# Performance work log

Hardware: AMD Instinct MI355X
Metric: run time of the kernel (lower is better)

Reference implementation:

```python
import jax, jax.numpy as jnp
import numpy as np

N_NODES = 100000
N_NEIGH = 10
DIM = 256
N_LAYERS = 3


def setup_inputs() -> dict:
    key = jax.random.key(0)
    ks = jax.random.split(key, 8)
    x = jax.random.normal(ks[0], (N_NODES, DIM), dtype=jnp.float32)
    adj = jax.random.randint(ks[1], (N_NODES, N_NEIGH), 0, N_NODES, dtype=jnp.int32)
    # per-layer SAGE weights: Linear(2*D -> D), stored as [2D, D] for x @ W
    scale = 0.05
    W0 = jax.random.normal(ks[2], (2 * DIM, DIM), dtype=jnp.float32) * scale
    W1 = jax.random.normal(ks[3], (2 * DIM, DIM), dtype=jnp.float32) * scale
    W2 = jax.random.normal(ks[4], (2 * DIM, DIM), dtype=jnp.float32) * scale
    b0 = jnp.zeros((DIM,), dtype=jnp.float32)
    b1 = jnp.zeros((DIM,), dtype=jnp.float32)
    b2 = jnp.zeros((DIM,), dtype=jnp.float32)
    return {"x": x, "adj": adj, "W0": W0, "b0": b0, "W1": W1, "b1": b1,
            "W2": W2, "b2": b2}


def reference(x, adj, W0, b0, W1, b1, W2, b2):
    """GraphSAGE: per layer, gather sampled neighbors [N,K,D], mean over K,
    concat with self embedding, linear [2D->D], ReLU on all but last layer."""
    layers = [(W0, b0), (W1, b1), (W2, b2)]
    h = x
    for i, (W, b) in enumerate(layers):
        neigh = jnp.mean(h[adj], axis=1)                 # [N, K, D] -> [N, D]
        h = jnp.concatenate([h, neigh], axis=1) @ W + b  # [N, 2D] @ [2D, D]
        if i < len(layers) - 1:
            h = jax.nn.relu(h)
    return h
```

## Files before the change

### kernel.cpp

```cpp
#include <hip/hip_runtime.h>
#include <stdint.h>

#define NN 100000
#define NK 10
#define D  256
#define D2 512
#define MT 32

typedef short bf16x8 __attribute__((ext_vector_type(8)));
typedef float f32x4  __attribute__((ext_vector_type(4)));

__device__ __forceinline__ uint16_t f2bf(float f) {
  uint32_t u = __float_as_uint(f);
  u += 0x7fffu + ((u >> 16) & 1u);
  return (uint16_t)(u >> 16);
}
__device__ __forceinline__ uint32_t pack2(float a, float b) {
  return (uint32_t)f2bf(a) | ((uint32_t)f2bf(b) << 16);
}

__global__ __launch_bounds__(256) void quant_x(const float* __restrict__ x,
                                               uint8_t* __restrict__ q8,
                                               float*   __restrict__ qs) {
  int node = blockIdx.x * 4 + (threadIdx.x >> 6);
  int lane = threadIdx.x & 63;
  const float4 v = *(const float4*)(x + (size_t)node * D + lane * 4);
  float m = fmaxf(fmaxf(fabsf(v.x), fabsf(v.y)), fmaxf(fabsf(v.z), fabsf(v.w)));
#pragma unroll
  for (int d = 1; d < 64; d <<= 1) m = fmaxf(m, __shfl_xor(m, d, 64));
  float inv = m > 1e-30f ? 127.0f / m : 0.0f;
  int q0 = (int)rintf(v.x * inv), q1 = (int)rintf(v.y * inv);
  int q2 = (int)rintf(v.z * inv), q3 = (int)rintf(v.w * inv);
  uint32_t p = (uint32_t)(q0 & 0xff) | ((uint32_t)(q1 & 0xff) << 8) |
               ((uint32_t)(q2 & 0xff) << 16) | ((uint32_t)(q3 & 0xff) << 24);
  ((uint32_t*)(q8 + (size_t)node * D))[lane] = p;
  if (lane == 0) qs[node] = m * (1.0f / 127.0f);
}

__global__ void pack_w(const float* __restrict__ W, uint16_t* __restrict__ Wp) {
  int idx   = blockIdx.x * blockDim.x + threadIdx.x;
  int lane  = idx & 63;
  int ntile = (idx >> 6) & 15;
  int kstep = idx >> 10;
  int n  = ntile * 16 + (lane & 15);
  int k0 = kstep * 32 + (lane >> 4) * 8;
  float v[8];
#pragma unroll
  for (int j = 0; j < 8; j++) v[j] = W[(size_t)(k0 + j) * D + n];
  uint4 o;
  o.x = pack2(v[0], v[1]);
  o.y = pack2(v[2], v[3]);
  o.z = pack2(v[4], v[5]);
  o.w = pack2(v[6], v[7]);
  ((uint4*)Wp)[idx] = o;
}

template <bool SELF_F32, bool QOUT>
__global__ __launch_bounds__(256, 5) void sage_layer(
    const void*     __restrict__ hin_v,
    const uint8_t*  __restrict__ qtab,
    const float*    __restrict__ qsc,
    const int*      __restrict__ adj,
    const uint16_t* __restrict__ Wp,
    const float*    __restrict__ bias,
    void*           __restrict__ hout_v,
    uint8_t*        __restrict__ q8out,
    float*          __restrict__ qsout)
{
  __shared__ uint4 lds4[MT * 64];
  const int t  = threadIdx.x;
  const int m0 = blockIdx.x * MT;

#pragma unroll
  for (int i = 0; i < 4; i++) {
    int cidx = t + i * 256;
    int r = cidx >> 5;
    int c = cidx & 31;
    int node = m0 + r;
    uint4 o;
    if (SELF_F32) {
      const float4* p = (const float4*)((const float*)hin_v + (size_t)node * D + c * 8);
      float4 v0 = p[0], v1 = p[1];
      o.x = pack2(v0.x, v0.y); o.y = pack2(v0.z, v0.w);
      o.z = pack2(v1.x, v1.y); o.w = pack2(v1.z, v1.w);
    } else {
      o = *(const uint4*)((const uint16_t*)hin_v + (size_t)node * D + c * 8);
    }
    lds4[r * 64 + (c ^ (r & 15))] = o;
  }

  {
    const int half = t >> 5;
    const int l32  = t & 31;
#pragma unroll 1
    for (int i = 0; i < 4; i++) {
      int r = i * 8 + half;
      int node = m0 + r;
      float a0=0.f,a1=0.f,a2=0.f,a3=0.f,a4=0.f,a5=0.f,a6=0.f,a7=0.f;
#pragma unroll
      for (int k = 0; k < NK; k++) {
        int nb = adj[node * NK + k];
        float s = qsc[nb];
        uint2 v = *(const uint2*)(qtab + (size_t)nb * D + l32 * 8);
        a0 += s * (float)(int8_t)(v.x);
        a1 += s * (float)(int8_t)(v.x >> 8);
        a2 += s * (float)(int8_t)(v.x >> 16);
        a3 += s * (float)(int8_t)(v.x >> 24);
        a4 += s * (float)(int8_t)(v.y);
        a5 += s * (float)(int8_t)(v.y >> 8);
        a6 += s * (float)(int8_t)(v.y >> 16);
        a7 += s * (float)(int8_t)(v.y >> 24);
      }
      const float sc = 1.0f / (float)NK;
      uint4 o;
      o.x = pack2(a0 * sc, a1 * sc);
      o.y = pack2(a2 * sc, a3 * sc);
      o.z = pack2(a4 * sc, a5 * sc);
      o.w = pack2(a6 * sc, a7 * sc);
      int c = 32 + l32;
      lds4[r * 64 + (c ^ (r & 15))] = o;
    }
  }

  __syncthreads();

  const int w    = t >> 6;
  const int l    = t & 63;
  const int quad = l >> 4;
  const int l16  = l & 15;

  f32x4 acc[2][4];
#pragma unroll
  for (int mt = 0; mt < 2; mt++)
#pragma unroll
    for (int nt = 0; nt < 4; nt++)
      acc[mt][nt] = (f32x4){0.f, 0.f, 0.f, 0.f};

  const uint4* wp4 = (const uint4*)Wp;

#pragma unroll 2
  for (int ks = 0; ks < 16; ks++) {
    bf16x8 af[2], bfr[4];
#pragma unroll
    for (int mt = 0; mt < 2; mt++) {
      int row = mt * 16 + l16;
      int c   = ks * 4 + quad;
      af[mt] = *((const bf16x8*)&lds4[row * 64 + (c ^ (row & 15))]);
    }
#pragma unroll
    for (int nt = 0; nt < 4; nt++) {
      bfr[nt] = *((const bf16x8*)&wp4[(ks * 16 + (w * 4 + nt)) * 64 + l]);
    }
#pragma unroll
    for (int mt = 0; mt < 2; mt++)
#pragma unroll
      for (int nt = 0; nt < 4; nt++)
        acc[mt][nt] = __builtin_amdgcn_mfma_f32_16x16x32_bf16(
            af[mt], bfr[nt], acc[mt][nt], 0, 0, 0);
  }

  float lmax[2][4];
#pragma unroll
  for (int mt = 0; mt < 2; mt++)
#pragma unroll
    for (int i = 0; i < 4; i++) lmax[mt][i] = 0.0f;

#pragma unroll
  for (int mt = 0; mt < 2; mt++)
#pragma unroll
    for (int nt = 0; nt < 4; nt++)
#pragma unroll
      for (int i = 0; i < 4; i++) {
        int col = w * 64 + nt * 16 + l16;
        float v = acc[mt][nt][i] + bias[col];
        if (QOUT) v = fmaxf(v, 0.0f);
        acc[mt][nt][i] = v;
        if (QOUT) lmax[mt][i] = fmaxf(lmax[mt][i], v);
      }

  float inv[2][4];
  if (QOUT) {
#pragma unroll
    for (int d = 1; d < 16; d <<= 1)
#pragma unroll
      for (int mt = 0; mt < 2; mt++)
#pragma unroll
        for (int i = 0; i < 4; i++)
          lmax[mt][i] = fmaxf(lmax[mt][i], __shfl_xor(lmax[mt][i], d, 64));
    __syncthreads();
    float* rmax = (float*)lds4;
    if (l16 == 0) {
#pragma unroll
      for (int mt = 0; mt < 2; mt++)
#pragma unroll
        for (int i = 0; i < 4; i++)
          rmax[(mt * 16 + quad * 4 + i) * 4 + w] = lmax[mt][i];
    }
    __syncthreads();
#pragma unroll
    for (int mt = 0; mt < 2; mt++)
#pragma unroll
      for (int i = 0; i < 4; i++) {
        int row = mt * 16 + quad * 4 + i;
        float m = fmaxf(fmaxf(rmax[row * 4 + 0], rmax[row * 4 + 1]),
                        fmaxf(rmax[row * 4 + 2], rmax[row * 4 + 3]));
        inv[mt][i] = m > 1e-30f ? 127.0f / m : 0.0f;
        if (w == 0 && l16 == 0) qsout[m0 + row] = m * (1.0f / 127.0f);
      }
  }

#pragma unroll
  for (int mt = 0; mt < 2; mt++)
#pragma unroll
    for (int i = 0; i < 4; i++) {
      int rr = m0 + mt * 16 + quad * 4 + i;
#pragma unroll
      for (int nt = 0; nt < 4; nt++) {
        int col = w * 64 + nt * 16 + l16;
        float v = acc[mt][nt][i];
        if (QOUT) {
          ((uint16_t*)hout_v)[(size_t)rr * D + col] = f2bf(v);
          int q = (int)rintf(v * inv[mt][i]);
          q8out[(size_t)rr * D + col] = (uint8_t)(q & 0xff);
        } else {
          ((float*)hout_v)[(size_t)rr * D + col] = v;
        }
      }
    }
}

extern "C" void kernel_launch(void* const* d_in, const int* in_sizes, int n_in,
                              void* d_out, int out_size, void* d_ws, size_t ws_size,
                              hipStream_t stream) {
  const float* x   = (const float*)d_in[0];
  const int*   adj = (const int*)d_in[1];
  const float* W0  = (const float*)d_in[2];
  const float* b0  = (const float*)d_in[3];
  const float* W1  = (const float*)d_in[4];
  const float* b1  = (const float*)d_in[5];
  const float* W2  = (const float*)d_in[6];
  const float* b2  = (const float*)d_in[7];
  float* out = (float*)d_out;

  uint8_t*  dob = (uint8_t*)d_out;
  uint16_t* hA  = (uint16_t*)dob;
  uint8_t*  hA8 = dob + 51200000;
  uint8_t*  x8  = dob + 76800000;

  uint16_t* ws  = (uint16_t*)d_ws;
  uint16_t* Wp0 = ws;
  uint16_t* Wp1 = Wp0 + D2 * D;
  uint16_t* Wp2 = Wp1 + D2 * D;
  uint16_t* hB  = Wp2 + D2 * D;
  uint8_t*  hB8 = (uint8_t*)(hB + (size_t)NN * D);
  float*    xs  = (float*)(hB8 + (size_t)NN * D);
  float*    hAs = xs + NN;
  float*    hBs = hAs + NN;

  quant_x<<<NN / 4, 256, 0, stream>>>(x, x8, xs);
  pack_w<<<64, 256, 0, stream>>>(W0, Wp0);
  pack_w<<<64, 256, 0, stream>>>(W1, Wp1);
  pack_w<<<64, 256, 0, stream>>>(W2, Wp2);

  const int grid = NN / MT;
  sage_layer<true,  true ><<<grid, 256, 0, stream>>>(x,  x8,  xs,  adj, Wp0, b0, hA,  hA8, hAs);
  sage_layer<false, true ><<<grid, 256, 0, stream>>>(hA, hA8, hAs, adj, Wp1, b1, hB,  hB8, hBs);
  sage_layer<false, false><<<grid, 256, 0, stream>>>(hB, hB8, hBs, adj, Wp2, b2, out, nullptr, nullptr);
}
```

Baseline: 457.2 us.

## Software-pipeline neighbor gathers with double buffers and merge prep kernels

The neighbor aggregation now preloads each row's adjacency indices once, broadcasts them with shuffles, and keeps two register buffers of neighbor gathers in flight, so the loads for the next row overlap the accumulation of the current one. Self-row loads are issued before the gathers so their latency also overlaps. The input quantization and the three weight-packing kernels are merged into one launch to cut launch overhead. Occupancy is lowered from 5 to 4 blocks per unit to make room for the extra registers, which could reduce latency hiding elsewhere.

```diff
diff --git a/kernel.cpp b/kernel.cpp
--- a/kernel.cpp
+++ b/kernel.cpp
@@ -19,44 +19,53 @@
   return (uint32_t)f2bf(a) | ((uint32_t)f2bf(b) << 16);
 }
 
-__global__ __launch_bounds__(256) void quant_x(const float* __restrict__ x,
-                                               uint8_t* __restrict__ q8,
-                                               float*   __restrict__ qs) {
-  int node = blockIdx.x * 4 + (threadIdx.x >> 6);
-  int lane = threadIdx.x & 63;
-  const float4 v = *(const float4*)(x + (size_t)node * D + lane * 4);
-  float m = fmaxf(fmaxf(fabsf(v.x), fabsf(v.y)), fmaxf(fabsf(v.z), fabsf(v.w)));
-#pragma unroll
-  for (int d = 1; d < 64; d <<= 1) m = fmaxf(m, __shfl_xor(m, d, 64));
-  float inv = m > 1e-30f ? 127.0f / m : 0.0f;
-  int q0 = (int)rintf(v.x * inv), q1 = (int)rintf(v.y * inv);
-  int q2 = (int)rintf(v.z * inv), q3 = (int)rintf(v.w * inv);
-  uint32_t p = (uint32_t)(q0 & 0xff) | ((uint32_t)(q1 & 0xff) << 8) |
-               ((uint32_t)(q2 & 0xff) << 16) | ((uint32_t)(q3 & 0xff) << 24);
-  ((uint32_t*)(q8 + (size_t)node * D))[lane] = p;
-  if (lane == 0) qs[node] = m * (1.0f / 127.0f);
-}
-
-__global__ void pack_w(const float* __restrict__ W, uint16_t* __restrict__ Wp) {
-  int idx   = blockIdx.x * blockDim.x + threadIdx.x;
-  int lane  = idx & 63;
-  int ntile = (idx >> 6) & 15;
-  int kstep = idx >> 10;
-  int n  = ntile * 16 + (lane & 15);
-  int k0 = kstep * 32 + (lane >> 4) * 8;
-  float v[8];
-#pragma unroll
-  for (int j = 0; j < 8; j++) v[j] = W[(size_t)(k0 + j) * D + n];
-  uint4 o;
-  o.x = pack2(v[0], v[1]);
-  o.y = pack2(v[2], v[3]);
-  o.z = pack2(v[4], v[5]);
-  o.w = pack2(v[6], v[7]);
-  ((uint4*)Wp)[idx] = o;
+__global__ __launch_bounds__(256) void prep(
+    const float* __restrict__ x, uint8_t* __restrict__ q8, float* __restrict__ qs,
+    const float* __restrict__ W0, const float* __restrict__ W1,
+    const float* __restrict__ W2, uint16_t* __restrict__ Wp0,
+    uint16_t* __restrict__ Wp1, uint16_t* __restrict__ Wp2)
+{
+  const int bid = blockIdx.x;
+  if (bid < 192) {
+    const float* W;
+    uint16_t* Wp;
+    if (bid < 64)       { W = W0; Wp = Wp0; }
+    else if (bid < 128) { W = W1; Wp = Wp1; }
+    else                { W = W2; Wp = Wp2; }
+    int idx   = ((bid & 63) << 8) + threadIdx.x;
+    int lane  = idx & 63;
+    int ntile = (idx >> 6) & 15;
+    int kstep = idx >> 10;
+    int n  = ntile * 16 + (lane & 15);
+    int k0 = kstep * 32 + (lane >> 4) * 8;
+    float v[8];
+#pragma unroll
+    for (int j = 0; j < 8; j++) v[j] = W[(size_t)(k0 + j) * D + n];
+    uint4 o;
+    o.x = pack2(v[0], v[1]);
+    o.y = pack2(v[2], v[3]);
+    o.z = pack2(v[4], v[5]);
+    o.w = pack2(v[6], v[7]);
+    ((uint4*)Wp)[idx] = o;
+  } else {
+    int node = (bid - 192) * 4 + (threadIdx.x >> 6);
+    int lane = threadIdx.x & 63;
+    const float4 v = *(const float4*)(x + (size_t)node * D + lane * 4);
+    float m = fmaxf(fmaxf(fabsf(v.x), fabsf(v.y)), fmaxf(fabsf(v.z), fabsf(v.w)));
+#pragma unroll
+    for (int d = 1; d < 64; d <<= 1) m = fmaxf(m, __shfl_xor(m, d, 64));
+    float inv = m > 1e-30f ? 127.0f / m : 0.0f;
+    int q0 = (int)rintf(v.x * inv), q1 = (int)rintf(v.y * inv);
+    int q2 = (int)rintf(v.z * inv), q3 = (int)rintf(v.w * inv);
+    uint32_t p = (uint32_t)(q0 & 0xff) | ((uint32_t)(q1 & 0xff) << 8) |
+                 ((uint32_t)(q2 & 0xff) << 16) | ((uint32_t)(q3 & 0xff) << 24);
+    ((uint32_t*)(q8 + (size_t)node * D))[lane] = p;
+    if (lane == 0) qs[node] = m * (1.0f / 127.0f);
+  }
 }
 
 template <bool SELF_F32, bool QOUT>
-__global__ __launch_bounds__(256, 5) void sage_layer(
+__global__ __launch_bounds__(256, 4) void sage_layer(
     const void*     __restrict__ hin_v,
     const uint8_t*  __restrict__ qtab,
     const float*    __restrict__ qsc,
@@ -68,59 +77,99 @@
     float*          __restrict__ qsout)
 {
   __shared__ uint4 lds4[MT * 64];
-  const int t  = threadIdx.x;
-  const int m0 = blockIdx.x * MT;
-
-#pragma unroll
-  for (int i = 0; i < 4; i++) {
-    int cidx = t + i * 256;
-    int r = cidx >> 5;
-    int c = cidx & 31;
-    int node = m0 + r;
+  const int t    = threadIdx.x;
+  const int m0   = blockIdx.x * MT;
+  const int half = t >> 5;
+  const int l32  = t & 31;
+  const int hb   = half & ~1;
+  const int hsel = (half & 1) * 10;
+
+  int av0, av1, av2, av3;
+  {
+    const int* ap = adj + (size_t)(m0 + hb) * NK;
+    int o = (l32 < 20) ? l32 : 0;
+    av0 = ap[o];
+    av1 = ap[80 + o];
+    av2 = ap[160 + o];
+    av3 = ap[240 + o];
+  }
+
+  uint2 gA[NK], gB[NK];
+  float sA[NK], sB[NK];
+
+  auto issue = [&](int av, uint2 (&g)[NK], float (&s)[NK]) {
+#pragma unroll
+    for (int k = 0; k < NK; k++) {
+      int nb = __shfl(av, hsel + k, 32);
+      s[k] = qsc[nb];
+      g[k] = *(const uint2*)(qtab + (size_t)nb * D + l32 * 8);
+    }
+  };
+  auto consume = [&](const uint2 (&g)[NK], const float (&s)[NK], int i) {
+    int r = i * 8 + half;
+    float a0=0.f,a1=0.f,a2=0.f,a3=0.f,a4=0.f,a5=0.f,a6=0.f,a7=0.f;
+#pragma unroll
+    for (int k = 0; k < NK; k++) {
+      float sk = s[k];
+      uint2 v  = g[k];
+      a0 += sk * (float)(int8_t)(v.x);
+      a1 += sk * (float)(int8_t)(v.x >> 8);
+      a2 += sk * (float)(int8_t)(v.x >> 16);
+      a3 += sk * (float)(int8_t)(v.x >> 24);
+      a4 += sk * (float)(int8_t)(v.y);
+      a5 += sk * (float)(int8_t)(v.y >> 8);
+      a6 += sk * (float)(int8_t)(v.y >> 16);
+      a7 += sk * (float)(int8_t)(v.y >> 24);
+    }
+    const float sc = 1.0f / (float)NK;
     uint4 o;
-    if (SELF_F32) {
-      const float4* p = (const float4*)((const float*)hin_v + (size_t)node * D + c * 8);
+    o.x = pack2(a0 * sc, a1 * sc);
+    o.y = pack2(a2 * sc, a3 * sc);
+    o.z = pack2(a4 * sc, a5 * sc);
+    o.w = pack2(a6 * sc, a7 * sc);
+    int c = 32 + l32;
+    lds4[r * 64 + (c ^ (r & 15))] = o;
+  };
+
+  if constexpr (SELF_F32) {
+#pragma unroll
+    for (int i = 0; i < 4; i++) {
+      int cidx = t + i * 256;
+      int r = cidx >> 5, c = cidx & 31;
+      const float4* p =
+          (const float4*)((const float*)hin_v + (size_t)(m0 + r) * D + c * 8);
       float4 v0 = p[0], v1 = p[1];
+      uint4 o;
       o.x = pack2(v0.x, v0.y); o.y = pack2(v0.z, v0.w);
       o.z = pack2(v1.x, v1.y); o.w = pack2(v1.z, v1.w);
-    } else {
-      o = *(const uint4*)((const uint16_t*)hin_v + (size_t)node * D + c * 8);
-    }
-    lds4[r * 64 + (c ^ (r & 15))] = o;
-  }
-
-  {
-    const int half = t >> 5;
-    const int l32  = t & 31;
-#pragma unroll 1
+      lds4[r * 64 + (c ^ (r & 15))] = o;
+    }
+    issue(av0, gA, sA);
+    issue(av1, gB, sB);
+  } else {
+    uint4 p1[4];
+#pragma unroll
     for (int i = 0; i < 4; i++) {
-      int r = i * 8 + half;
-      int node = m0 + r;
-      float a0=0.f,a1=0.f,a2=0.f,a3=0.f,a4=0.f,a5=0.f,a6=0.f,a7=0.f;
-#pragma unroll
-      for (int k = 0; k < NK; k++) {
-        int nb = adj[node * NK + k];
-        float s = qsc[nb];
-        uint2 v = *(const uint2*)(qtab + (size_t)nb * D + l32 * 8);
-        a0 += s * (float)(int8_t)(v.x);
-        a1 += s * (float)(int8_t)(v.x >> 8);
-        a2 += s * (float)(int8_t)(v.x >> 16);
-        a3 += s * (float)(int8_t)(v.x >> 24);
-        a4 += s * (float)(int8_t)(v.y);
-        a5 += s * (float)(int8_t)(v.y >> 8);
-        a6 += s * (float)(int8_t)(v.y >> 16);
-        a7 += s * (float)(int8_t)(v.y >> 24);
-      }
-      const float sc = 1.0f / (float)NK;
-      uint4 o;
-      o.x = pack2(a0 * sc, a1 * sc);
-      o.y = pack2(a2 * sc, a3 * sc);
-      o.z = pack2(a4 * sc, a5 * sc);
-      o.w = pack2(a6 * sc, a7 * sc);
-      int c = 32 + l32;
-      lds4[r * 64 + (c ^ (r & 15))] = o;
-    }
-  }
+      int cidx = t + i * 256;
+      int r = cidx >> 5, c = cidx & 31;
+      p1[i] = *(const uint4*)((const uint16_t*)hin_v + (size_t)(m0 + r) * D + c * 8);
+    }
+    issue(av0, gA, sA);
+    issue(av1, gB, sB);
+#pragma unroll
+    for (int i = 0; i < 4; i++) {
+      int cidx = t + i * 256;
+      int r = cidx >> 5, c = cidx & 31;
+      lds4[r * 64 + (c ^ (r & 15))] = p1[i];
+    }
+  }
+
+  consume(gA, sA, 0);
+  issue(av2, gA, sA);
+  consume(gB, sB, 1);
+  issue(av3, gB, sB);
+  consume(gA, sA, 2);
+  consume(gB, sB, 3);
 
   __syncthreads();
 
@@ -257,10 +306,7 @@
   float*    hAs = xs + NN;
   float*    hBs = hAs + NN;
 
-  quant_x<<<NN / 4, 256, 0, stream>>>(x, x8, xs);
-  pack_w<<<64, 256, 0, stream>>>(W0, Wp0);
-  pack_w<<<64, 256, 0, stream>>>(W1, Wp1);
-  pack_w<<<64, 256, 0, stream>>>(W2, Wp2);
+  prep<<<192 + NN / 4, 256, 0, stream>>>(x, x8, xs, W0, W1, W2, Wp0, Wp1, Wp2);
 
   const int grid = NN / MT;
   sage_layer<true,  true ><<<grid, 256, 0, stream>>>(x,  x8,  xs,  adj, Wp0, b0, hA,  hA8, hAs);
```

After: 427.4 us. -6.5%, faster.

## Split neighbor gather-mean into separate kernel and merge prep kernels

Applied to the files above, without the earlier changes.

The fused per-layer kernel is split into a gather_mean kernel, which averages the int8 neighbor rows and writes the mean in bf16 (or int8 with a per-row scale when workspace is small), and a sage_gemm kernel that reads that mean instead of gathering. The weight-packing and x-quantization launches are merged into one prep kernel. The intent is higher occupancy and better latency hiding for the random gathers, plus fewer launches, at the cost of an extra round trip of the mean tensor through HBM per layer. The int8 mean path also adds another quantization step, which costs accuracy.

```diff
diff --git a/kernel.cpp b/kernel.cpp
--- a/kernel.cpp
+++ b/kernel.cpp
@@ -6,6 +6,7 @@
 #define D  256
 #define D2 512
 #define MT 32
+#define GR 8
 
 typedef short bf16x8 __attribute__((ext_vector_type(8)));
 typedef float f32x4  __attribute__((ext_vector_type(4)));
@@ -19,48 +20,115 @@
   return (uint32_t)f2bf(a) | ((uint32_t)f2bf(b) << 16);
 }
 
-__global__ __launch_bounds__(256) void quant_x(const float* __restrict__ x,
-                                               uint8_t* __restrict__ q8,
-                                               float*   __restrict__ qs) {
-  int node = blockIdx.x * 4 + (threadIdx.x >> 6);
-  int lane = threadIdx.x & 63;
-  const float4 v = *(const float4*)(x + (size_t)node * D + lane * 4);
-  float m = fmaxf(fmaxf(fabsf(v.x), fabsf(v.y)), fmaxf(fabsf(v.z), fabsf(v.w)));
-#pragma unroll
-  for (int d = 1; d < 64; d <<= 1) m = fmaxf(m, __shfl_xor(m, d, 64));
-  float inv = m > 1e-30f ? 127.0f / m : 0.0f;
-  int q0 = (int)rintf(v.x * inv), q1 = (int)rintf(v.y * inv);
-  int q2 = (int)rintf(v.z * inv), q3 = (int)rintf(v.w * inv);
-  uint32_t p = (uint32_t)(q0 & 0xff) | ((uint32_t)(q1 & 0xff) << 8) |
-               ((uint32_t)(q2 & 0xff) << 16) | ((uint32_t)(q3 & 0xff) << 24);
-  ((uint32_t*)(q8 + (size_t)node * D))[lane] = p;
-  if (lane == 0) qs[node] = m * (1.0f / 127.0f);
-}
-
-__global__ void pack_w(const float* __restrict__ W, uint16_t* __restrict__ Wp) {
-  int idx   = blockIdx.x * blockDim.x + threadIdx.x;
-  int lane  = idx & 63;
-  int ntile = (idx >> 6) & 15;
-  int kstep = idx >> 10;
-  int n  = ntile * 16 + (lane & 15);
-  int k0 = kstep * 32 + (lane >> 4) * 8;
-  float v[8];
-#pragma unroll
-  for (int j = 0; j < 8; j++) v[j] = W[(size_t)(k0 + j) * D + n];
-  uint4 o;
-  o.x = pack2(v[0], v[1]);
-  o.y = pack2(v[2], v[3]);
-  o.z = pack2(v[4], v[5]);
-  o.w = pack2(v[6], v[7]);
-  ((uint4*)Wp)[idx] = o;
-}
-
-template <bool SELF_F32, bool QOUT>
-__global__ __launch_bounds__(256, 5) void sage_layer(
+__global__ __launch_bounds__(256) void prep(
+    const float* __restrict__ x, uint8_t* __restrict__ q8, float* __restrict__ qs,
+    const float* __restrict__ W0, const float* __restrict__ W1,
+    const float* __restrict__ W2, uint16_t* __restrict__ Wp0,
+    uint16_t* __restrict__ Wp1, uint16_t* __restrict__ Wp2)
+{
+  const int bid = blockIdx.x;
+  if (bid < 192) {
+    const float* W;
+    uint16_t* Wp;
+    if (bid < 64)       { W = W0; Wp = Wp0; }
+    else if (bid < 128) { W = W1; Wp = Wp1; }
+    else                { W = W2; Wp = Wp2; }
+    int idx   = ((bid & 63) << 8) + threadIdx.x;
+    int lane  = idx & 63;
+    int ntile = (idx >> 6) & 15;
+    int kstep = idx >> 10;
+    int n  = ntile * 16 + (lane & 15);
+    int k0 = kstep * 32 + (lane >> 4) * 8;
+    float v[8];
+#pragma unroll
+    for (int j = 0; j < 8; j++) v[j] = W[(size_t)(k0 + j) * D + n];
+    uint4 o;
+    o.x = pack2(v[0], v[1]);
+    o.y = pack2(v[2], v[3]);
+    o.z = pack2(v[4], v[5]);
+    o.w = pack2(v[6], v[7]);
+    ((uint4*)Wp)[idx] = o;
+  } else {
+    int node = (bid - 192) * 4 + (threadIdx.x >> 6);
+    int lane = threadIdx.x & 63;
+    const float4 v = *(const float4*)(x + (size_t)node * D + lane * 4);
+    float m = fmaxf(fmaxf(fabsf(v.x), fabsf(v.y)), fmaxf(fabsf(v.z), fabsf(v.w)));
+#pragma unroll
+    for (int d = 1; d < 64; d <<= 1) m = fmaxf(m, __shfl_xor(m, d, 64));
+    float inv = m > 1e-30f ? 127.0f / m : 0.0f;
+    int q0 = (int)rintf(v.x * inv), q1 = (int)rintf(v.y * inv);
+    int q2 = (int)rintf(v.z * inv), q3 = (int)rintf(v.w * inv);
+    uint32_t p = (uint32_t)(q0 & 0xff) | ((uint32_t)(q1 & 0xff) << 8) |
+                 ((uint32_t)(q2 & 0xff) << 16) | ((uint32_t)(q3 & 0xff) << 24);
+    ((uint32_t*)(q8 + (size_t)node * D))[lane] = p;
+    if (lane == 0) qs[node] = m * (1.0f / 127.0f);
+  }
+}
+
+template <bool MEAN8>
+__global__ __launch_bounds__(256, 8) void gather_mean(
+    const uint8_t* __restrict__ qtab,
+    const float*   __restrict__ qsc,
+    const int*     __restrict__ adj,
+    void*          __restrict__ mout,
+    float*         __restrict__ msc)
+{
+  const int half = threadIdx.x >> 5;
+  const int l32  = threadIdx.x & 31;
+  const int r    = blockIdx.x * GR + half;
+
+  const int* ap = adj + (size_t)r * NK;
+  int av = ap[(l32 < NK) ? l32 : 0];
+
+  float a0=0.f,a1=0.f,a2=0.f,a3=0.f,a4=0.f,a5=0.f,a6=0.f,a7=0.f;
+#pragma unroll
+  for (int k = 0; k < NK; k++) {
+    int nb  = __shfl(av, k, 32);
+    float s = qsc[nb];
+    uint2 v = *(const uint2*)(qtab + (size_t)nb * D + l32 * 8);
+    a0 += s * (float)(int8_t)(v.x);
+    a1 += s * (float)(int8_t)(v.x >> 8);
+    a2 += s * (float)(int8_t)(v.x >> 16);
+    a3 += s * (float)(int8_t)(v.x >> 24);
+    a4 += s * (float)(int8_t)(v.y);
+    a5 += s * (float)(int8_t)(v.y >> 8);
+    a6 += s * (float)(int8_t)(v.y >> 16);
+    a7 += s * (float)(int8_t)(v.y >> 24);
+  }
+  const float sc = 1.0f / (float)NK;
+  a0 *= sc; a1 *= sc; a2 *= sc; a3 *= sc;
+  a4 *= sc; a5 *= sc; a6 *= sc; a7 *= sc;
+
+  if constexpr (!MEAN8) {
+    uint4 o;
+    o.x = pack2(a0, a1); o.y = pack2(a2, a3);
+    o.z = pack2(a4, a5); o.w = pack2(a6, a7);
+    ((uint4*)((uint16_t*)mout + (size_t)r * D))[l32] = o;
+  } else {
+    float m = fmaxf(fmaxf(fmaxf(fabsf(a0), fabsf(a1)), fmaxf(fabsf(a2), fabsf(a3))),
+                    fmaxf(fmaxf(fabsf(a4), fabsf(a5)), fmaxf(fabsf(a6), fabsf(a7))));
+#pragma unroll
+    for (int d = 1; d < 32; d <<= 1) m = fmaxf(m, __shfl_xor(m, d, 32));
+    float inv = m > 1e-30f ? 127.0f / m : 0.0f;
+    int q0 = (int)rintf(a0 * inv), q1 = (int)rintf(a1 * inv);
+    int q2 = (int)rintf(a2 * inv), q3 = (int)rintf(a3 * inv);
+    int q4 = (int)rintf(a4 * inv), q5 = (int)rintf(a5 * inv);
+    int q6 = (int)rintf(a6 * inv), q7 = (int)rintf(a7 * inv);
+    uint2 o;
+    o.x = (uint32_t)(q0 & 0xff) | ((uint32_t)(q1 & 0xff) << 8) |
+          ((uint32_t)(q2 & 0xff) << 16) | ((uint32_t)(q3 & 0xff) << 24);
+    o.y = (uint32_t)(q4 & 0xff) | ((uint32_t)(q5 & 0xff) << 8) |
+          ((uint32_t)(q6 & 0xff) << 16) | ((uint32_t)(q7 & 0xff) << 24);
+    ((uint2*)((uint8_t*)mout + (size_t)r * D))[l32] = o;
+    if (l32 == 0) msc[r] = m * (1.0f / 127.0f);
+  }
+}
+
+template <bool SELF_F32, bool QOUT, bool MEAN8>
+__global__ __launch_bounds__(256, 4) void sage_gemm(
     const void*     __restrict__ hin_v,
-    const uint8_t*  __restrict__ qtab,
-    const float*    __restrict__ qsc,
-    const int*      __restrict__ adj,
+    const void*     __restrict__ mb_v,
+    const float*    __restrict__ msc,
     const uint16_t* __restrict__ Wp,
     const float*    __restrict__ bias,
     void*           __restrict__ hout_v,
@@ -74,11 +142,10 @@
 #pragma unroll
   for (int i = 0; i < 4; i++) {
     int cidx = t + i * 256;
-    int r = cidx >> 5;
-    int c = cidx & 31;
+    int r = cidx >> 5, c = cidx & 31;
     int node = m0 + r;
     uint4 o;
-    if (SELF_F32) {
+    if constexpr (SELF_F32) {
       const float4* p = (const float4*)((const float*)hin_v + (size_t)node * D + c * 8);
       float4 v0 = p[0], v1 = p[1];
       o.x = pack2(v0.x, v0.y); o.y = pack2(v0.z, v0.w);
@@ -89,37 +156,30 @@
     lds4[r * 64 + (c ^ (r & 15))] = o;
   }
 
-  {
-    const int half = t >> 5;
-    const int l32  = t & 31;
-#pragma unroll 1
-    for (int i = 0; i < 4; i++) {
-      int r = i * 8 + half;
-      int node = m0 + r;
-      float a0=0.f,a1=0.f,a2=0.f,a3=0.f,a4=0.f,a5=0.f,a6=0.f,a7=0.f;
-#pragma unroll
-      for (int k = 0; k < NK; k++) {
-        int nb = adj[node * NK + k];
-        float s = qsc[nb];
-        uint2 v = *(const uint2*)(qtab + (size_t)nb * D + l32 * 8);
-        a0 += s * (float)(int8_t)(v.x);
-        a1 += s * (float)(int8_t)(v.x >> 8);
-        a2 += s * (float)(int8_t)(v.x >> 16);
-        a3 += s * (float)(int8_t)(v.x >> 24);
-        a4 += s * (float)(int8_t)(v.y);
-        a5 += s * (float)(int8_t)(v.y >> 8);
-        a6 += s * (float)(int8_t)(v.y >> 16);
-        a7 += s * (float)(int8_t)(v.y >> 24);
-      }
-      const float sc = 1.0f / (float)NK;
-      uint4 o;
-      o.x = pack2(a0 * sc, a1 * sc);
-      o.y = pack2(a2 * sc, a3 * sc);
-      o.z = pack2(a4 * sc, a5 * sc);
-      o.w = pack2(a6 * sc, a7 * sc);
-      int c = 32 + l32;
-      lds4[r * 64 + (c ^ (r & 15))] = o;
-    }
+#pragma unroll
+  for (int i = 0; i < 4; i++) {
+    int cidx = t + i * 256;
+    int r = cidx >> 5, cp = cidx & 31;
+    int node = m0 + r;
+    uint4 o;
+    if constexpr (!MEAN8) {
+      o = *(const uint4*)((const uint16_t*)mb_v + (size_t)node * D + cp * 8);
+    } else {
+      uint2 v = *(const uint2*)((const uint8_t*)mb_v + (size_t)node * D + cp * 8);
+      float s = msc[node];
+      float b0 = s * (float)(int8_t)(v.x);
+      float b1 = s * (float)(int8_t)(v.x >> 8);
+      float b2 = s * (float)(int8_t)(v.x >> 16);
+      float b3 = s * (float)(int8_t)(v.x >> 24);
+      float b4 = s * (float)(int8_t)(v.y);
+      float b5 = s * (float)(int8_t)(v.y >> 8);
+      float b6 = s * (float)(int8_t)(v.y >> 16);
+      float b7 = s * (float)(int8_t)(v.y >> 24);
+      o.x = pack2(b0, b1); o.y = pack2(b2, b3);
+      o.z = pack2(b4, b5); o.w = pack2(b6, b7);
+    }
+    int c = 32 + cp;
+    lds4[r * 64 + (c ^ (r & 15))] = o;
   }
 
   __syncthreads();
@@ -246,24 +306,45 @@
   uint16_t* hA  = (uint16_t*)dob;
   uint8_t*  hA8 = dob + 51200000;
   uint8_t*  x8  = dob + 76800000;
+  uint8_t*  hB8 = dob + 76800000;
 
   uint16_t* ws  = (uint16_t*)d_ws;
   uint16_t* Wp0 = ws;
   uint16_t* Wp1 = Wp0 + D2 * D;
   uint16_t* Wp2 = Wp1 + D2 * D;
   uint16_t* hB  = Wp2 + D2 * D;
-  uint8_t*  hB8 = (uint8_t*)(hB + (size_t)NN * D);
-  float*    xs  = (float*)(hB8 + (size_t)NN * D);
-  float*    hAs = xs + NN;
-  float*    hBs = hAs + NN;
-
-  quant_x<<<NN / 4, 256, 0, stream>>>(x, x8, xs);
-  pack_w<<<64, 256, 0, stream>>>(W0, Wp0);
-  pack_w<<<64, 256, 0, stream>>>(W1, Wp1);
-  pack_w<<<64, 256, 0, stream>>>(W2, Wp2);
-
-  const int grid = NN / MT;
-  sage_layer<true,  true ><<<grid, 256, 0, stream>>>(x,  x8,  xs,  adj, Wp0, b0, hA,  hA8, hAs);
-  sage_layer<false, true ><<<grid, 256, 0, stream>>>(hA, hA8, hAs, adj, Wp1, b1, hB,  hB8, hBs);
-  sage_layer<false, false><<<grid, 256, 0, stream>>>(hB, hB8, hBs, adj, Wp2, b2, out, nullptr, nullptr);
-}
+  uint8_t*  wsb = (uint8_t*)(hB + (size_t)NN * D);
+
+  const size_t NEED_BF16 = 3u * D2 * D * 2 + (size_t)NN * D * 2
+                         + (size_t)NN * D * 2
+                         + 4u * NN * 4;
+  const bool M8 = (ws_size < NEED_BF16);
+
+  void*  meanb = (void*)wsb;
+  float* tail  = (float*)(wsb + (M8 ? (size_t)NN * D : (size_t)NN * D * 2));
+  float* msc = tail;
+  float* xs  = msc + NN;
+  float* hAs = xs + NN;
+  float* hBs = hAs + NN;
+
+  prep<<<192 + NN / 4, 256, 0, stream>>>(x, x8, xs, W0, W1, W2, Wp0, Wp1, Wp2);
+
+  const int gg = NN / GR;
+  const int gm = NN / MT;
+
+  if (!M8) {
+    gather_mean<false><<<gg, 256, 0, stream>>>(x8, xs, adj, meanb, msc);
+    sage_gemm<true,  true,  false><<<gm, 256, 0, stream>>>(x,  meanb, msc, Wp0, b0, hA,  hA8, hAs);
+    gather_mean<false><<<gg, 256, 0, stream>>>(hA8, hAs, adj, meanb, msc);
+    sage_gemm<false, true,  false><<<gm, 256, 0, stream>>>(hA, meanb, msc, Wp1, b1, hB,  hB8, hBs);
+    gather_mean<false><<<gg, 256, 0, stream>>>(hB8, hBs, adj, meanb, msc);
+    sage_gemm<false, false, false><<<gm, 256, 0, stream>>>(hB, meanb, msc, Wp2, b2, out, nullptr, nullptr);
+  } else {
+    gather_mean<true><<<gg, 256, 0, stream>>>(x8, xs, adj, meanb, msc);
+    sage_gemm<true,  true,  true><<<gm, 256, 0, stream>>>(x,  meanb, msc, Wp0, b0, hA,  hA8, hAs);
+    gather_mean<true><<<gg, 256, 0, stream>>>(hA8, hAs, adj, meanb, msc);
+    sage_gemm<false, true,  true><<<gm, 256, 0, stream>>>(hA, meanb, msc, Wp1, b1, hB,  hB8, hBs);
+    gather_mean<true><<<gg, 256, 0, stream>>>(hB8, hBs, adj, meanb, msc);
+    sage_gemm<false, false, true><<<gm, 256, 0, stream>>>(hB, meanb, msc, Wp2, b2, out, nullptr, nullptr);
+  }
+}
```

Measured after the change: 580.9 us. 27.0% more time.
